# Kernel optimization log

Measured on AMD Instinct MI355X. Metric: run time of the kernel, lower is better.

The kernel has to match this reference:

```python
import jax, jax.numpy as jnp
import numpy as np

BN_EPS = 1e-5
STRIDE = 4
K_NEAREST = 16


def _fps(xyz, m):
    """Farthest point sampling. xyz: [n,3] -> indices [m] (seeded at point 0)."""
    n = xyz.shape[0]

    def body(i, state):
        dist, idxs, last = state
        d = jnp.sum((xyz - xyz[last]) ** 2, axis=-1)
        dist = jnp.minimum(dist, d)
        nxt = jnp.argmax(dist).astype(jnp.int32)
        return dist, idxs.at[i].set(nxt), nxt

    init = (jnp.full((n,), 1e10, xyz.dtype), jnp.zeros((m,), jnp.int32), jnp.int32(0))
    _, idxs, _ = jax.lax.fori_loop(1, m, body, init)
    return idxs


def _knn(q, x, k):
    """q: [m,3] queries, x: [n,3] points -> [m,k] nearest-neighbor indices."""
    d = jnp.sum((q[:, None, :] - x[None, :, :]) ** 2, axis=-1)  # [m,n]
    _, idx = jax.lax.top_k(-d, k)
    return idx


def setup_inputs() -> dict:
    key = jax.random.key(0)
    k0, k1, k2 = jax.random.split(key, 3)
    B, N, IN_CH, OUT_CH = 4, 8192, 64, 128
    events = jax.random.uniform(k0, (B, N, 4), dtype=jnp.float32)  # xyz in [0,1) + time
    features = jax.random.normal(k1, (B, N, IN_CH), dtype=jnp.float32)
    W = jax.random.normal(k2, (4 + IN_CH, OUT_CH), dtype=jnp.float32) / np.float32(np.sqrt(4 + IN_CH))
    b = jnp.zeros((OUT_CH,), jnp.float32)
    gamma = jnp.ones((OUT_CH,), jnp.float32)
    beta = jnp.zeros((OUT_CH,), jnp.float32)
    return dict(events=events, features=features, W=W, b=b, gamma=gamma, beta=beta)


def reference(events, features, W, b, gamma, beta):
    B, N, _ = events.shape
    m = N // STRIDE  # down_offsets = offsets // stride with equal-size samples
    xyz = events[..., :3]
    xyz_c = jax.lax.stop_gradient(xyz)  # indices are non-differentiable

    # farthest point sampling per cloud -> [B, m]
    down_idx = jax.vmap(lambda p: _fps(p, m))(xyz_c)
    down_xyz = jnp.take_along_axis(xyz_c, down_idx[..., None], axis=1)  # [B,m,3]
    # k nearest neighbors of each sampled point -> [B, m, K]
    idx = jax.vmap(lambda q, x: _knn(q, x, K_NEAREST))(down_xyz, xyz_c)

    down_events = jnp.take_along_axis(events, down_idx[..., None], axis=1)  # [B,m,4]
    grouped_events = jax.vmap(lambda e, i: e[i])(events, idx)               # [B,m,K,4]
    grouped_events_norm = grouped_events - down_events[:, :, None, :]
    grouped_features = jax.vmap(lambda f, i: f[i])(features, idx)           # [B,m,K,in_ch]
    g = jnp.concatenate([grouped_events_norm, grouped_features], axis=-1)   # [B,m,K,4+in_ch]

    # Linear -> BatchNorm1d (training batch stats over all points & neighbors) -> ReLU
    h = jnp.einsum('bmkc,cd->bmkd', g, W) + b
    mu = jnp.mean(h, axis=(0, 1, 2))
    var = jnp.var(h, axis=(0, 1, 2))
    h = (h - mu) * jax.lax.rsqrt(var + BN_EPS) * gamma + beta
    h = jax.nn.relu(h)

    down_features = jnp.max(h, axis=2)  # max-pool over K neighbors -> [B,m,out_ch]
    return down_events, down_features
```

## Files before the change

### kernel.cpp

```cpp
#include <hip/hip_runtime.h>

#define N_PTS 8192
#define M_PTS 2048
#define K_NN 16
#define IN_CH 64
#define G_CH 68
#define OUT_CH 128
#define KCAP 128

__device__ __forceinline__ float subrn(float a, float b) {
    float r; asm("v_sub_f32 %0, %1, %2" : "=v"(r) : "v"(a), "v"(b)); return r;
}
__device__ __forceinline__ float mulrn(float a, float b) {
    float r; asm("v_mul_f32 %0, %1, %2" : "=v"(r) : "v"(a), "v"(b)); return r;
}
__device__ __forceinline__ float addrn(float a, float b) {
    float r; asm("v_add_f32 %0, %1, %2" : "=v"(r) : "v"(a), "v"(b)); return r;
}
__device__ __forceinline__ float sqdist_rn(float ax, float ay, float az,
                                           float bx, float by, float bz) {
    float dx = subrn(ax, bx);
    float dy = subrn(ay, by);
    float dz = subrn(az, bz);
    return addrn(addrn(mulrn(dx, dx), mulrn(dy, dy)), mulrn(dz, dz));
}

typedef float v2f __attribute__((ext_vector_type(2)));
__device__ __forceinline__ v2f pk_add(v2f a, v2f b) {
    v2f r; asm("v_pk_add_f32 %0, %1, %2" : "=v"(r) : "v"(a), "v"(b)); return r;
}
__device__ __forceinline__ v2f pk_mul(v2f a, v2f b) {
    v2f r; asm("v_pk_mul_f32 %0, %1, %2" : "=v"(r) : "v"(a), "v"(b)); return r;
}

template <int CTRL>
__device__ __forceinline__ float movdpp_f(float x) {
    int r = __builtin_amdgcn_mov_dpp(__float_as_int(x), CTRL, 0xf, 0xf, true);
    return __int_as_float(r);
}
template <int CTRL, int RM>
__device__ __forceinline__ float dppmaxf_m(float x) {
    int r = __builtin_amdgcn_update_dpp(0, __float_as_int(x), CTRL, RM, 0xf, false);
    return fmaxf(x, __int_as_float(r));
}
__device__ __forceinline__ float wave_max64(float x) {
    x = fmaxf(x, movdpp_f<0xB1>(x));
    x = fmaxf(x, movdpp_f<0x4E>(x));
    x = fmaxf(x, movdpp_f<0x141>(x));
    x = fmaxf(x, movdpp_f<0x140>(x));
    x = dppmaxf_m<0x142, 0xa>(x);
    x = dppmaxf_m<0x143, 0xc>(x);
    return x;
}
__device__ __forceinline__ float group8_max(float x) {
    x = fmaxf(x, movdpp_f<0xB1>(x));
    x = fmaxf(x, movdpp_f<0x4E>(x));
    x = fmaxf(x, movdpp_f<0x141>(x));
    return x;
}

__global__ __launch_bounds__(512, 2) void fps_kernel(const float4* __restrict__ events4,
                                                     int* __restrict__ down_idx,
                                                     float4* __restrict__ out_de) {
    extern __shared__ char smem[];
    float*  rv   = (float*)smem;
    int*    wsl  = (int*)(smem + 32);
    int*    ssel = (int*)(smem + 64);
    float4* spt  = (float4*)(smem + 64 + 4 * M_PTS);

    const int b = blockIdx.x;
    const int tid = threadIdx.x;
    const int wave = tid >> 6;
    const int lane = tid & 63;
    const float4* ev = events4 + (size_t)b * N_PTS;

    for (int i = tid; i < N_PTS; i += 512) spt[i] = ev[i];
    if (tid == 0) { ssel[0] = 0; wsl[0] = 0x7fffffff; wsl[1] = 0x7fffffff; }
    __syncthreads();

    v2f px[8], py[8], pz[8];
    float dist[16];
#pragma unroll
    for (int pp = 0; pp < 8; ++pp) {
        float4 f0 = spt[(2 * pp) * 512 + tid];
        float4 f1 = spt[(2 * pp + 1) * 512 + tid];
        px[pp] = (v2f){f0.x, f1.x};
        py[pp] = (v2f){f0.y, f1.y};
        pz[pp] = (v2f){f0.z, f1.z};
        dist[2 * pp] = 1e10f; dist[2 * pp + 1] = 1e10f;
    }

    int last = 0;
    for (int i = 1; i < M_PTS; ++i) {
        float4 L = spt[last];
        const float nlx = -L.x, nly = -L.y, nlz = -L.z;
        const v2f nx2 = (v2f){nlx, nlx};
        const v2f ny2 = (v2f){nly, nly};
        const v2f nz2 = (v2f){nlz, nlz};
#pragma unroll
        for (int pp = 0; pp < 8; ++pp) {
            v2f dx = pk_add(px[pp], nx2);
            v2f dy = pk_add(py[pp], ny2);
            v2f dz = pk_add(pz[pp], nz2);
            v2f s  = pk_add(pk_add(pk_mul(dx, dx), pk_mul(dy, dy)), pk_mul(dz, dz));
            dist[2 * pp]     = fminf(dist[2 * pp],     s.x);
            dist[2 * pp + 1] = fminf(dist[2 * pp + 1], s.y);
        }
        float t0[8];
#pragma unroll
        for (int j = 0; j < 8; ++j) t0[j] = fmaxf(dist[2 * j], dist[2 * j + 1]);
#pragma unroll
        for (int j = 0; j < 4; ++j) t0[j] = fmaxf(t0[2 * j], t0[2 * j + 1]);
        float bd = fmaxf(fmaxf(t0[0], t0[1]), fmaxf(t0[2], t0[3]));

        float wm = wave_max64(bd);
        if (lane == 63) rv[wave] = wm;
        __syncthreads();
        float bm = group8_max(rv[lane & 7]);

        if (bd == bm) {
            int jm = 0;
#pragma unroll
            for (int j = 15; j >= 0; --j) if (dist[j] == bd) jm = j;
            atomicMin(&wsl[i & 1], jm * 512 + tid);
        }
        __syncthreads();
        last = wsl[i & 1];
        if (tid == 0) { ssel[i] = last; wsl[(i + 1) & 1] = 0x7fffffff; }
    }
    __syncthreads();

    for (int i = tid; i < M_PTS; i += 512) {
        int s = ssel[i];
        down_idx[b * M_PTS + i] = s;
        out_de[(size_t)b * M_PTS + i] = spt[s];
    }
}

__global__ __launch_bounds__(256, 1) void knn_kernel(const float4* __restrict__ events4,
                                                     const int* __restrict__ down_idx,
                                                     int* __restrict__ knn_idx) {
    extern __shared__ char smem[];
    float2* sxy  = (float2*)smem;
    float*  sz   = (float*)(smem + N_PTS * 8);
    float*  cd   = sz + N_PTS;
    int*    ci   = (int*)(cd + 32 * KCAP);
    int*    scnt = (int*)(ci + 32 * KCAP);

    const int b    = blockIdx.x >> 6;
    const int qg   = blockIdx.x & 63;
    const int tid  = threadIdx.x;
    const int ql   = tid >> 3;
    const int part = tid & 7;

    const float4* ev = events4 + (size_t)b * N_PTS;
    for (int i = tid; i < N_PTS; i += 256) {
        float4 e = ev[i];
        sxy[i] = (float2){e.x, e.y}; sz[i] = e.z;
    }
    if (tid < 32) scnt[tid] = 0;
    __syncthreads();

    const int q  = qg * 32 + ql;
    const int qi = down_idx[b * M_PTS + q];
    const float2 qxy = sxy[qi];
    const float qx = qxy.x, qy = qxy.y, qz = sz[qi];

    const float4* sxy4 = (const float4*)sxy;
    const float2* sz2  = (const float2*)sz;

    float m1 = 1e30f, m2 = 1e30f;
    for (int i = 0; i < N_PTS / 16; ++i) {
        const int ph = i * 8 + part;
        float4 xy = sxy4[ph];
        float2 zz = sz2[ph];
        float d0 = sqdist_rn(xy.x, xy.y, zz.x, qx, qy, qz);
        float d1 = sqdist_rn(xy.z, xy.w, zz.y, qx, qy, qz);
        float lo0 = fminf(m1, d0);
        m2 = fminf(m2, fmaxf(m1, d0));
        m1 = lo0;
        float lo1 = fminf(m1, d1);
        m2 = fminf(m2, fmaxf(m1, d1));
        m1 = lo1;
    }
    const float T = group8_max(m2);

    for (int i = 0; i < N_PTS / 16; ++i) {
        const int ph = i * 8 + part;
        float4 xy = sxy4[ph];
        float2 zz = sz2[ph];
        float d0 = sqdist_rn(xy.x, xy.y, zz.x, qx, qy, qz);
        float d1 = sqdist_rn(xy.z, xy.w, zz.y, qx, qy, qz);
        if (d0 <= T) {
            int pos = atomicAdd(&scnt[ql], 1);
            if (pos < KCAP) { cd[ql * KCAP + pos] = d0; ci[ql * KCAP + pos] = 2 * ph; }
        }
        if (d1 <= T) {
            int pos = atomicAdd(&scnt[ql], 1);
            if (pos < KCAP) { cd[ql * KCAP + pos] = d1; ci[ql * KCAP + pos] = 2 * ph + 1; }
        }
    }
    __syncthreads();

    if (part == 0) {
        float nd[16]; int ni[16];
#pragma unroll
        for (int j = 0; j < 16; ++j) { nd[j] = 1e30f; ni[j] = 0x7fffffff; }
        float wmax = 1e30f; int widx = 0x7fffffff; int wslot = 0;
        const int n = scnt[ql];
        const int lim = (n <= KCAP) ? n : 0;
        for (int t = 0; t < lim; ++t) {
            float d = cd[ql * KCAP + t];
            int   p = ci[ql * KCAP + t];
            if (d < wmax || (d == wmax && p < widx)) {
#pragma unroll
                for (int j = 0; j < 16; ++j) if (j == wslot) { nd[j] = d; ni[j] = p; }
                float m_ = -1.0f; int mix_ = -1; int ms_ = 0;
#pragma unroll
                for (int j = 0; j < 16; ++j)
                    if (nd[j] > m_ || (nd[j] == m_ && ni[j] > mix_)) { m_ = nd[j]; mix_ = ni[j]; ms_ = j; }
                wmax = m_; widx = mix_; wslot = ms_;
            }
        }
        if (n > KCAP) {
            for (int p = 0; p < N_PTS; ++p) {
                float2 pxy = sxy[p];
                float d = sqdist_rn(pxy.x, pxy.y, sz[p], qx, qy, qz);
                if (d < wmax || (d == wmax && p < widx)) {
#pragma unroll
                    for (int j = 0; j < 16; ++j) if (j == wslot) { nd[j] = d; ni[j] = p; }
                    float m_ = -1.0f; int mix_ = -1; int ms_ = 0;
#pragma unroll
                    for (int j = 0; j < 16; ++j)
                        if (nd[j] > m_ || (nd[j] == m_ && ni[j] > mix_)) { m_ = nd[j]; mix_ = ni[j]; ms_ = j; }
                    wmax = m_; widx = mix_; wslot = ms_;
                }
            }
        }
        int* out = knn_idx + ((size_t)(b * M_PTS + q)) * K_NN;
#pragma unroll
        for (int j = 0; j < 16; ++j) out[j] = ni[j];
    }
}

__global__ __launch_bounds__(256, 2) void gmm_kernel(const float4* __restrict__ events4,
                                                     const float4* __restrict__ feat4,
                                                     const float* __restrict__ W,
                                                     const float* __restrict__ bias,
                                                     const int* __restrict__ knn_idx,
                                                     const float4* __restrict__ de4,
                                                     float* __restrict__ hmax_g,
                                                     float* __restrict__ hmin_g,
                                                     float* __restrict__ gsum,
                                                     float* __restrict__ gsq) {
    __shared__ __align__(16) float4 sg4[2 * 16 * 17];
    __shared__ float scomb[2 * OUT_CH];

    const int b   = blockIdx.x >> 7;
    const int qg  = blockIdx.x & 127;
    const int tid = threadIdx.x;
    const int d   = tid & 127;
    const int qs  = tid >> 7;

    float w[G_CH];
#pragma unroll
    for (int c = 0; c < G_CH; ++c) w[c] = W[c * OUT_CH + d];
    const float breg = bias[d];

    float ssum = 0.f, ssq = 0.f;

    for (int r = 0; r < 8; ++r) {
        const int base = b * M_PTS + qg * 16 + 2 * r;
        for (int j4 = tid; j4 < 2 * 16 * 17; j4 += 256) {
            int qq = j4 / 272;
            int rem = j4 - qq * 272;
            int k = rem / 17;
            int c4 = rem - k * 17;
            int nb = knn_idx[(base + qq) * K_NN + k];
            float4 v;
            if (c4 == 0) {
                float4 e = events4[(size_t)b * N_PTS + nb];
                float4 d0 = de4[base + qq];
                v = (float4){e.x - d0.x, e.y - d0.y, e.z - d0.z, e.w - d0.w};
            } else {
                v = feat4[((size_t)(b * N_PTS + nb)) * 16 + (c4 - 1)];
            }
            sg4[j4] = v;
        }
        __syncthreads();

        float hmax = -1e30f, hmin = 1e30f;
#pragma unroll
        for (int k = 0; k < 16; ++k) {
            float acc = breg;
#pragma unroll
            for (int c4 = 0; c4 < 17; ++c4) {
                float4 g = sg4[qs * 272 + k * 17 + c4];
                acc = fmaf(g.x, w[4 * c4 + 0], acc);
                acc = fmaf(g.y, w[4 * c4 + 1], acc);
                acc = fmaf(g.z, w[4 * c4 + 2], acc);
                acc = fmaf(g.w, w[4 * c4 + 3], acc);
            }
            hmax = fmaxf(hmax, acc);
            hmin = fminf(hmin, acc);
            ssum += acc;
            ssq = fmaf(acc, acc, ssq);
        }
        const size_t o = (size_t)(base + qs) * OUT_CH + d;
        hmax_g[o] = hmax;
        hmin_g[o] = hmin;
        __syncthreads();
    }

    if (qs == 1) { scomb[d] = ssum; scomb[OUT_CH + d] = ssq; }
    __syncthreads();
    if (qs == 0) {
        atomicAdd(&gsum[d], ssum + scomb[d]);
        atomicAdd(&gsq[d],  ssq  + scomb[OUT_CH + d]);
    }
}

__global__ __launch_bounds__(256) void fin_kernel(const float* __restrict__ hmax_g,
                                                  const float* __restrict__ hmin_g,
                                                  const float* __restrict__ gsum,
                                                  const float* __restrict__ gsq,
                                                  const float* __restrict__ gamma,
                                                  const float* __restrict__ beta,
                                                  float* __restrict__ out) {
    const size_t e = (size_t)blockIdx.x * 256 + threadIdx.x;
    const int d = (int)(e & 127);
    const float inv_cnt = 1.0f / 131072.0f;
    float mu  = gsum[d] * inv_cnt;
    float var = gsq[d] * inv_cnt - mu * mu;
    float a   = gamma[d] * rsqrtf(var + 1e-5f);
    float sh  = fmaf(-mu, a, beta[d]);
    float hv  = (a >= 0.f) ? hmax_g[e] : hmin_g[e];
    float r   = fmaf(a, hv, sh);
    out[32768 + e] = r > 0.f ? r : 0.f;
}

extern "C" void kernel_launch(void* const* d_in, const int* in_sizes, int n_in,
                              void* d_out, int out_size, void* d_ws, size_t ws_size,
                              hipStream_t stream) {
    const float* events   = (const float*)d_in[0];
    const float* features = (const float*)d_in[1];
    const float* W        = (const float*)d_in[2];
    const float* bias     = (const float*)d_in[3];
    const float* gamma    = (const float*)d_in[4];
    const float* beta     = (const float*)d_in[5];
    float* out = (float*)d_out;
    char* ws = (char*)d_ws;

    int*   down_idx = (int*)ws;
    int*   knn_idx  = (int*)(ws + 32768);
    float* gsum     = (float*)(ws + 32768 + 524288);
    float* gsq      = gsum + OUT_CH;
    float* hmaxg    = (float*)(ws + 558080);
    float* hming    = hmaxg + (size_t)4 * M_PTS * OUT_CH;

    (void)hipMemsetAsync(gsum, 0, 2 * OUT_CH * sizeof(float), stream);

    const size_t fps_lds = 64 + 4 * M_PTS + (size_t)N_PTS * sizeof(float4);
    fps_kernel<<<4, 512, fps_lds, stream>>>((const float4*)events, down_idx, (float4*)out);

    const size_t knn_lds = (size_t)N_PTS * 8 + (size_t)N_PTS * 4
                         + (size_t)32 * KCAP * 8 + 128;
    knn_kernel<<<256, 256, knn_lds, stream>>>((const float4*)events, down_idx, knn_idx);

    gmm_kernel<<<512, 256, 0, stream>>>((const float4*)events, (const float4*)features,
                                        W, bias, knn_idx, (const float4*)out,
                                        hmaxg, hming, gsum, gsq);

    fin_kernel<<<4096, 256, 0, stream>>>(hmaxg, hming, gsum, gsq, gamma, beta, out);
}
```

Before: 2.392 ms.

## Use packed 64-bit atomicMax argmax to drop one barrier per FPS iteration

Replaces the two-barrier FPS argmax (per-wave max written to LDS, barrier, group max, then atomicMin on index) with a single-barrier scheme. Each wave's best candidates atomically max a packed key that holds the float distance in the high bits and the inverted index in the low bits. A triple-buffered slot is reset one iteration ahead, so the reset cannot race with the read. This removes one __syncthreads per iteration across 2047 serial iterations, at the cost of more lanes issuing 64-bit LDS atomics.

```diff
diff --git a/kernel.cpp b/kernel.cpp
--- a/kernel.cpp
+++ b/kernel.cpp
@@ -63,19 +63,19 @@
                                                      int* __restrict__ down_idx,
                                                      float4* __restrict__ out_de) {
     extern __shared__ char smem[];
-    float*  rv   = (float*)smem;
-    int*    wsl  = (int*)(smem + 32);
-    int*    ssel = (int*)(smem + 64);
-    float4* spt  = (float4*)(smem + 64 + 4 * M_PTS);
+    unsigned long long* wslot = (unsigned long long*)smem;
+    int*    ssel = (int*)(smem + 32);
+    float4* spt  = (float4*)(smem + 32 + 4 * M_PTS);
 
     const int b = blockIdx.x;
     const int tid = threadIdx.x;
-    const int wave = tid >> 6;
-    const int lane = tid & 63;
     const float4* ev = events4 + (size_t)b * N_PTS;
 
     for (int i = tid; i < N_PTS; i += 512) spt[i] = ev[i];
-    if (tid == 0) { ssel[0] = 0; wsl[0] = 0x7fffffff; wsl[1] = 0x7fffffff; }
+    if (tid == 0) {
+        ssel[0] = 0;
+        wslot[0] = 0ull; wslot[1] = 0ull; wslot[2] = 0ull;
+    }
     __syncthreads();
 
     v2f px[8], py[8], pz[8];
@@ -114,19 +114,23 @@
         float bd = fmaxf(fmaxf(t0[0], t0[1]), fmaxf(t0[2], t0[3]));
 
         float wm = wave_max64(bd);
-        if (lane == 63) rv[wave] = wm;
-        __syncthreads();
-        float bm = group8_max(rv[lane & 7]);
+        float bm = __int_as_float(__builtin_amdgcn_readlane(__float_as_int(wm), 63));
 
         if (bd == bm) {
             int jm = 0;
 #pragma unroll
             for (int j = 15; j >= 0; --j) if (dist[j] == bd) jm = j;
-            atomicMin(&wsl[i & 1], jm * 512 + tid);
-        }
+            unsigned int pid = (unsigned int)(jm * 512 + tid);
+            unsigned long long key =
+                ((unsigned long long)__float_as_uint(bd) << 32)
+              | (unsigned long long)(0xFFFFFFFFu - pid);
+            atomicMax(&wslot[i % 3], key);
+        }
+        if (tid == 0) wslot[(i + 1) % 3] = 0ull;
         __syncthreads();
-        last = wsl[i & 1];
-        if (tid == 0) { ssel[i] = last; wsl[(i + 1) & 1] = 0x7fffffff; }
+        unsigned long long wk = wslot[i % 3];
+        last = (int)(0xFFFFFFFFu - (unsigned int)wk);
+        if (tid == 0) ssel[i] = last;
     }
     __syncthreads();
 
@@ -206,7 +210,7 @@
         float nd[16]; int ni[16];
 #pragma unroll
         for (int j = 0; j < 16; ++j) { nd[j] = 1e30f; ni[j] = 0x7fffffff; }
-        float wmax = 1e30f; int widx = 0x7fffffff; int wslot = 0;
+        float wmax = 1e30f; int widx = 0x7fffffff; int wslot_ = 0;
         const int n = scnt[ql];
         const int lim = (n <= KCAP) ? n : 0;
         for (int t = 0; t < lim; ++t) {
@@ -214,12 +218,12 @@
             int   p = ci[ql * KCAP + t];
             if (d < wmax || (d == wmax && p < widx)) {
 #pragma unroll
-                for (int j = 0; j < 16; ++j) if (j == wslot) { nd[j] = d; ni[j] = p; }
+                for (int j = 0; j < 16; ++j) if (j == wslot_) { nd[j] = d; ni[j] = p; }
                 float m_ = -1.0f; int mix_ = -1; int ms_ = 0;
 #pragma unroll
                 for (int j = 0; j < 16; ++j)
                     if (nd[j] > m_ || (nd[j] == m_ && ni[j] > mix_)) { m_ = nd[j]; mix_ = ni[j]; ms_ = j; }
-                wmax = m_; widx = mix_; wslot = ms_;
+                wmax = m_; widx = mix_; wslot_ = ms_;
             }
         }
         if (n > KCAP) {
@@ -228,12 +232,12 @@
                 float d = sqdist_rn(pxy.x, pxy.y, sz[p], qx, qy, qz);
                 if (d < wmax || (d == wmax && p < widx)) {
 #pragma unroll
-                    for (int j = 0; j < 16; ++j) if (j == wslot) { nd[j] = d; ni[j] = p; }
+                    for (int j = 0; j < 16; ++j) if (j == wslot_) { nd[j] = d; ni[j] = p; }
                     float m_ = -1.0f; int mix_ = -1; int ms_ = 0;
 #pragma unroll
                     for (int j = 0; j < 16; ++j)
                         if (nd[j] > m_ || (nd[j] == m_ && ni[j] > mix_)) { m_ = nd[j]; mix_ = ni[j]; ms_ = j; }
-                    wmax = m_; widx = mix_; wslot = ms_;
+                    wmax = m_; widx = mix_; wslot_ = ms_;
                 }
             }
         }
@@ -360,7 +364,7 @@
 
     (void)hipMemsetAsync(gsum, 0, 2 * OUT_CH * sizeof(float), stream);
 
-    const size_t fps_lds = 64 + 4 * M_PTS + (size_t)N_PTS * sizeof(float4);
+    const size_t fps_lds = 32 + 4 * M_PTS + (size_t)N_PTS * sizeof(float4);
     fps_kernel<<<4, 512, fps_lds, stream>>>((const float4*)events, down_idx, (float4*)out);
 
     const size_t knn_lds = (size_t)N_PTS * 8 + (size_t)N_PTS * 4
```

Result: slower. 2.605 ms (+8.9%).
